# Kernel optimization log

Hardware: AMD Instinct MI355X
Metric: run time of the kernel (lower is better)

Reference implementation:

```python
import jax, jax.numpy as jnp
import numpy as np

B, S = 32, 2048
D = 128      # embedding_dim
H = 256      # hidden_dim
K = 512      # codebook_size
RECON_COEF, COMMIT_COEF, VQ_COEF = 1.0, 0.15, 0.05


def _conv1d(x, w, b):
    # x: [B, Cin, S], w: [Cout, Cin, 3], 'SAME' padding (padding=1, k=3)
    y = jax.lax.conv_general_dilated(x, w, window_strides=(1,), padding='SAME',
                                     dimension_numbers=('NCH', 'OIH', 'NCH'))
    return y + b[None, :, None]


def _lrelu(x):
    return jnp.where(x >= 0, x, 0.2 * x)


def setup_inputs() -> dict:
    key = jax.random.key(0)
    ks = jax.random.split(key, 14)

    def w(k, shape, fan_in):
        bound = 1.0 / np.sqrt(fan_in)
        return jax.random.uniform(k, shape, jnp.float32, -bound, bound)

    return {
        'x': jax.random.normal(ks[0], (B, S), jnp.float32),
        'codebook': jax.random.normal(ks[1], (K, D), jnp.float32),
        'ew1': w(ks[2], (H, 1, 3), 1 * 3),  'eb1': w(ks[3], (H,), 1 * 3),
        'ew2': w(ks[4], (H, H, 3), H * 3),  'eb2': w(ks[5], (H,), H * 3),
        'ew3': w(ks[6], (D, H, 3), H * 3),  'eb3': w(ks[7], (D,), H * 3),
        'dw1': w(ks[8], (H, D, 3), D * 3),  'db1': w(ks[9], (H,), D * 3),
        'dw2': w(ks[10], (H, H, 3), H * 3), 'db2': w(ks[11], (H,), H * 3),
        'dw3': w(ks[12], (1, H, 3), H * 3), 'db3': w(ks[13], (1,), H * 3),
    }


def reference(x, codebook, ew1, eb1, ew2, eb2, ew3, eb3, dw1, db1, dw2, db2, dw3, db3):
    # ---- encode ----
    h = x[:, None, :]                                  # [B,1,S]
    h = _lrelu(_conv1d(h, ew1, eb1))
    h = _lrelu(_conv1d(h, ew2, eb2))
    z = _conv1d(h, ew3, eb3)                           # [B,D,S]

    # ---- vector quantize (eval mode: no EMA update) ----
    zt = jnp.transpose(z, (0, 2, 1))                   # [B,S,D]
    z_flat = zt.reshape(-1, D)                         # [B*S,D]
    # squared distances: |z|^2 + |c|^2 - 2 z c^T
    d = (jnp.sum(z_flat ** 2, axis=1, keepdims=True)
         + jnp.sum(codebook ** 2, axis=1)
         - 2.0 * z_flat @ codebook.T)                  # [B*S,K]
    idx = jnp.argmin(d, axis=1)                        # [B*S]
    z_q = codebook[idx].reshape(zt.shape)              # [B,S,D] (== one-hot @ codebook)

    vq_loss = jnp.mean((jax.lax.stop_gradient(zt) - z_q) ** 2) * VQ_COEF
    commitment_loss = jnp.mean((zt - jax.lax.stop_gradient(z_q)) ** 2) * COMMIT_COEF
    indices = idx.reshape(B, S)

    # ---- decode ----
    h = jnp.transpose(z_q, (0, 2, 1))                  # [B,D,S]
    h = _lrelu(_conv1d(h, dw1, db1))
    h = _lrelu(_conv1d(h, dw2, db2))
    x_recon = _conv1d(h, dw3, db3)[:, 0, :]            # [B,S]

    recon_loss = jnp.mean((x - x_recon) ** 2) * RECON_COEF
    loss = recon_loss + vq_loss + commitment_loss
    return x_recon, indices, loss, recon_loss, vq_loss, commitment_loss
```

## Files before the change

### kernel.cpp

```cpp
#include <hip/hip_runtime.h>
#include <float.h>

#define S_LEN 2048
#define BATCH 32
#define HCH   256
#define DCH   128
#define KCODES 512

typedef float  f32x4  __attribute__((ext_vector_type(4)));
typedef short  bf16x8 __attribute__((ext_vector_type(8)));
typedef short  short8 __attribute__((ext_vector_type(8)));

__device__ __forceinline__ float lrelu_f(float v) { return v >= 0.f ? v : 0.2f * v; }

__device__ __forceinline__ short f2bf(float f) {
    unsigned u = __float_as_uint(f);
    u = u + 0x7fffu + ((u >> 16) & 1u);
    return (short)(u >> 16);
}
__device__ __forceinline__ float bf2f(unsigned short u) {
    return __uint_as_float(((unsigned)u) << 16);
}

__global__ void prep_cb_split_kernel(const float* __restrict__ cb,
                                     short* __restrict__ cb_hi, short* __restrict__ cb_lo,
                                     float* __restrict__ cnorm) {
    int k = blockIdx.x * 256 + threadIdx.x;
    if (k < KCODES) {
        float s = 0.f;
        for (int d = 0; d < DCH; ++d) {
            float v = cb[k * DCH + d];
            s += v * v;
            short hi = f2bf(v);
            short lo = f2bf(v - bf2f((unsigned short)hi));
            cb_hi[k * DCH + d] = hi;
            cb_lo[k * DCH + d] = lo;
        }
        cnorm[k] = s;
    }
}

__global__ void prep_w_split_kernel(const float* __restrict__ Wsrc,
                                    short* __restrict__ Wh, short* __restrict__ Wl,
                                    int Cout, int Cin) {
    int i = blockIdx.x * 256 + threadIdx.x;
    int total = 3 * Cout * Cin;
    if (i < total) {
        int t = i / (Cout * Cin);
        int rem = i - t * Cout * Cin;
        int co = rem / Cin;
        int ci = rem - co * Cin;
        float v = Wsrc[(co * Cin + ci) * 3 + t];
        short hi = f2bf(v);
        Wh[i] = hi;
        Wl[i] = f2bf(v - bf2f((unsigned short)hi));
    }
}

__global__ void prep_wdec_kernel(const float* __restrict__ Wsrc, short* __restrict__ Wdst,
                                 int Cin) {
    int i = blockIdx.x * 256 + threadIdx.x;
    int total = 3 * 256 * Cin;
    if (i < total) {
        int t = i / (256 * Cin);
        int rem = i - t * 256 * Cin;
        int co = rem / Cin;
        int ci = rem - co * Cin;
        Wdst[i] = f2bf(Wsrc[(co * Cin + ci) * 3 + t]);
    }
}

__global__ void prep_w3t_kernel(const float* __restrict__ w3, float* __restrict__ w3t) {
    int i = blockIdx.x * 256 + threadIdx.x;
    if (i < 768) {
        int t = i / 256, ci = i - t * 256;
        w3t[i] = w3[ci * 3 + t];
    }
}

__global__ __launch_bounds__(256) void enc_conv1_cl_kernel(
        const float* __restrict__ x, short* __restrict__ h_hi, short* __restrict__ h_lo,
        const float* __restrict__ w, const float* __restrict__ bias) {
    __shared__ float ws[HCH * 3];
    __shared__ float bs[HCH];
    int tid = threadIdx.x;
    for (int i = tid; i < HCH * 3; i += 256) ws[i] = w[i];
    for (int i = tid; i < HCH; i += 256) bs[i] = bias[i];
    __syncthreads();
    int b = blockIdx.y;
    int s = blockIdx.x * 32 + (tid >> 3);
    int cch = tid & 7;
    const float* xb = x + (size_t)b * S_LEN;
    float xm = (s > 0) ? xb[s - 1] : 0.f;
    float x0 = xb[s];
    float xp = (s < S_LEN - 1) ? xb[s + 1] : 0.f;
    size_t base = ((size_t)(b * S_LEN + s)) * HCH + cch * 32;
#pragma unroll
    for (int cc = 0; cc < 4; ++cc) {
        short8 oh, ol;
#pragma unroll
        for (int e = 0; e < 8; ++e) {
            int co = cch * 32 + cc * 8 + e;
            float v = ws[co * 3 + 0] * xm + ws[co * 3 + 1] * x0 + ws[co * 3 + 2] * xp + bs[co];
            v = lrelu_f(v);
            short hi = f2bf(v);
            oh[e] = hi;
            ol[e] = f2bf(v - bf2f((unsigned short)hi));
        }
        *(short8*)(h_hi + base + cc * 8) = oh;
        *(short8*)(h_lo + base + cc * 8) = ol;
    }
}

__global__ __launch_bounds__(256) void conv_mfma_split(
        const short* __restrict__ in_hi, const short* __restrict__ in_lo,
        short* __restrict__ out_hi, short* __restrict__ out_lo,
        const short* __restrict__ wt_hi, const short* __restrict__ wt_lo,
        const float* __restrict__ bias, int Cin, int Cout, int do_lrelu) {
    __shared__ short smem[20800];
    short* Xh = smem;
    short* Xl = smem + 130 * 40;

    const int tid = threadIdx.x;
    const int lane = tid & 63;
    const int w = tid >> 6;
    const int m = lane & 15;
    const int q = lane >> 4;
    const int sOff = (w & 1) * 64;
    const int cOff = (w >> 1) * 64;
    const int b = blockIdx.z;
    const int s0 = blockIdx.x * 128;
    const int co0 = blockIdx.y * 128;

    f32x4 acc[4][4];
    f32x4 zero4 = {0.f, 0.f, 0.f, 0.f};
#pragma unroll
    for (int i = 0; i < 4; ++i)
#pragma unroll
        for (int j = 0; j < 4; ++j) acc[i][j] = zero4;

    const short* inhb = in_hi + (size_t)b * S_LEN * Cin;
    const short* inlb = in_lo + (size_t)b * S_LEN * Cin;

    for (int ci0 = 0; ci0 < Cin; ci0 += 32) {
        __syncthreads();
        for (int c = tid; c < 520; c += 256) {
            int r = c >> 2, part = c & 3;
            int s = s0 - 1 + r;
            float4 vh = make_float4(0.f, 0.f, 0.f, 0.f);
            float4 vl = vh;
            if (s >= 0 && s < S_LEN) {
                size_t goff = (size_t)s * Cin + ci0 + part * 8;
                vh = *(const float4*)(inhb + goff);
                vl = *(const float4*)(inlb + goff);
            }
            *(float4*)(Xh + r * 40 + part * 8) = vh;
            *(float4*)(Xl + r * 40 + part * 8) = vl;
        }
        __syncthreads();

#pragma unroll
        for (int t = 0; t < 3; ++t) {
            bf16x8 ah[4], al[4], bh[4], bl[4];
#pragma unroll
            for (int i = 0; i < 4; ++i) {
                int row = sOff + i * 16 + m + t;
                ah[i] = *(const bf16x8*)(Xh + row * 40 + q * 8);
                al[i] = *(const bf16x8*)(Xl + row * 40 + q * 8);
            }
#pragma unroll
            for (int j = 0; j < 4; ++j) {
                size_t woff = ((size_t)(t * Cout + co0 + cOff + j * 16 + m)) * Cin + ci0 + q * 8;
                bh[j] = *(const bf16x8*)(wt_hi + woff);
                bl[j] = *(const bf16x8*)(wt_lo + woff);
            }
#pragma unroll
            for (int i = 0; i < 4; ++i)
#pragma unroll
                for (int j = 0; j < 4; ++j) {
                    acc[i][j] = __builtin_amdgcn_mfma_f32_16x16x32_bf16(ah[i], bh[j], acc[i][j], 0, 0, 0);
                    acc[i][j] = __builtin_amdgcn_mfma_f32_16x16x32_bf16(ah[i], bl[j], acc[i][j], 0, 0, 0);
                    acc[i][j] = __builtin_amdgcn_mfma_f32_16x16x32_bf16(al[i], bh[j], acc[i][j], 0, 0, 0);
                }
        }
    }

    short* obH = smem + w * 5120;
    short* obL = obH + 2560;
#pragma unroll
    for (int p = 0; p < 2; ++p) {
        __syncthreads();
#pragma unroll
        for (int jj = 0; jj < 2; ++jj) {
            int j = 2 * p + jj;
            float bv = bias[co0 + cOff + j * 16 + m];
#pragma unroll
            for (int i = 0; i < 4; ++i) {
#pragma unroll
                for (int r = 0; r < 4; ++r) {
                    float val = acc[i][j][r] + bv;
                    if (do_lrelu) val = lrelu_f(val);
                    short hi = f2bf(val);
                    short lo = f2bf(val - bf2f((unsigned short)hi));
                    int row = i * 16 + q * 4 + r;
                    int col = jj * 16 + m;
                    obH[row * 40 + col] = hi;
                    obL[row * 40 + col] = lo;
                }
            }
        }
        __syncthreads();
        const int chunk = lane & 3;
        const int rsub = lane >> 2;
#pragma unroll
        for (int it = 0; it < 4; ++it) {
            int row = it * 16 + rsub;
            short8 vh = *(const short8*)(obH + row * 40 + chunk * 8);
            short8 vl = *(const short8*)(obL + row * 40 + chunk * 8);
            size_t goff = ((size_t)(b * S_LEN + s0 + sOff + row)) * Cout + co0 + cOff + p * 32 + chunk * 8;
            *(short8*)(out_hi + goff) = vh;
            *(short8*)(out_lo + goff) = vl;
        }
    }
}

__global__ __launch_bounds__(256) void vq_mfma_kernel(
        const short* __restrict__ z_hi, const short* __restrict__ z_lo,
        const short* __restrict__ cb_hi, const short* __restrict__ cb_lo,
        const float* __restrict__ cnorm, int* __restrict__ idx_out,
        float* __restrict__ idx_f_out) {
    __shared__ short smem[2 * 64 * 136];
    __shared__ float redv[64][4];
    __shared__ int   redi[64][4];
    short* Zh = smem;
    short* Zl = smem + 64 * 136;

    const int tid = threadIdx.x;
    const int lane = tid & 63;
    const int w = tid >> 6;
    const int m = lane & 15;
    const int q = lane >> 4;
    const int n0 = blockIdx.x * 64;

    for (int c = tid; c < 2048; c += 256) {
        int buf = c >> 10;
        int rem = c & 1023;
        int r = rem >> 4, part = rem & 15;
        size_t goff = (size_t)(n0 + r) * DCH + part * 8;
        float4 v = buf ? *(const float4*)(z_lo + goff) : *(const float4*)(z_hi + goff);
        *(float4*)((buf ? Zl : Zh) + r * 136 + part * 8) = v;
    }
    __syncthreads();

    float best[4][4];
    int besti[4][4];
#pragma unroll
    for (int i = 0; i < 4; ++i)
#pragma unroll
        for (int r = 0; r < 4; ++r) { best[i][r] = FLT_MAX; besti[i][r] = 0; }

    for (int k0 = 0; k0 < KCODES; k0 += 256) {
        f32x4 acc[4][4];
        f32x4 zero4 = {0.f, 0.f, 0.f, 0.f};
#pragma unroll
        for (int i = 0; i < 4; ++i)
#pragma unroll
            for (int j = 0; j < 4; ++j) acc[i][j] = zero4;

#pragma unroll
        for (int d0 = 0; d0 < DCH; d0 += 32) {
            bf16x8 ah[4], al[4], bh[4], bl[4];
#pragma unroll
            for (int i = 0; i < 4; ++i) {
                int row = i * 16 + m;
                ah[i] = *(const bf16x8*)(Zh + row * 136 + d0 + q * 8);
                al[i] = *(const bf16x8*)(Zl + row * 136 + d0 + q * 8);
            }
#pragma unroll
            for (int j = 0; j < 4; ++j) {
                size_t coff = (size_t)(k0 + w * 64 + j * 16 + m) * DCH + d0 + q * 8;
                bh[j] = *(const bf16x8*)(cb_hi + coff);
                bl[j] = *(const bf16x8*)(cb_lo + coff);
            }
#pragma unroll
            for (int i = 0; i < 4; ++i)
#pragma unroll
                for (int j = 0; j < 4; ++j) {
                    acc[i][j] = __builtin_amdgcn_mfma_f32_16x16x32_bf16(ah[i], bh[j], acc[i][j], 0, 0, 0);
                    acc[i][j] = __builtin_amdgcn_mfma_f32_16x16x32_bf16(ah[i], bl[j], acc[i][j], 0, 0, 0);
                    acc[i][j] = __builtin_amdgcn_mfma_f32_16x16x32_bf16(al[i], bh[j], acc[i][j], 0, 0, 0);
                }
        }
#pragma unroll
        for (int j = 0; j < 4; ++j) {
            int k = k0 + w * 64 + j * 16 + m;
            float cn = cnorm[k];
#pragma unroll
            for (int i = 0; i < 4; ++i)
#pragma unroll
                for (int r = 0; r < 4; ++r) {
                    float dv = cn - 2.f * acc[i][j][r];
                    if (dv < best[i][r]) { best[i][r] = dv; besti[i][r] = k; }
                }
        }
    }

#pragma unroll
    for (int mask = 1; mask < 16; mask <<= 1) {
#pragma unroll
        for (int i = 0; i < 4; ++i)
#pragma unroll
            for (int r = 0; r < 4; ++r) {
                float ov = __shfl_xor(best[i][r], mask);
                int oi = __shfl_xor(besti[i][r], mask);
                if (ov < best[i][r] || (ov == best[i][r] && oi < besti[i][r])) {
                    best[i][r] = ov; besti[i][r] = oi;
                }
            }
    }
    if (m == 0) {
#pragma unroll
        for (int i = 0; i < 4; ++i)
#pragma unroll
            for (int r = 0; r < 4; ++r) {
                int srow = i * 16 + q * 4 + r;
                redv[srow][w] = best[i][r];
                redi[srow][w] = besti[i][r];
            }
    }
    __syncthreads();
    if (tid < 64) {
        float bv = redv[tid][0];
        int bi = redi[tid][0];
#pragma unroll
        for (int w2 = 1; w2 < 4; ++w2) {
            float v = redv[tid][w2];
            int ii = redi[tid][w2];
            if (v < bv || (v == bv && ii < bi)) { bv = v; bi = ii; }
        }
        int n = n0 + tid;
        idx_out[n] = bi;
        idx_f_out[n] = (float)bi;
    }
}

__global__ __launch_bounds__(256) void gather_vqsum_kernel(
        const float* __restrict__ cb, const int* __restrict__ idxb,
        const short* __restrict__ z_hi, const short* __restrict__ z_lo,
        short* __restrict__ zq, float* __restrict__ acc_vq) {
    int tid = threadIdx.x;
    int b = blockIdx.y;
    int s = blockIdx.x * 32 + (tid >> 3);
    int dpart = tid & 7;
    int n = b * S_LEN + s;
    int k = idxb[n];
    const float* src = cb + (size_t)k * DCH + dpart * 16;
    size_t zoff = (size_t)n * DCH + dpart * 16;
    float sum = 0.f;
    short8 outv[2];
#pragma unroll
    for (int half = 0; half < 2; ++half) {
        float4 f0 = *(const float4*)(src + half * 8);
        float4 f1 = *(const float4*)(src + half * 8 + 4);
        bf16x8 zh = *(const bf16x8*)(z_hi + zoff + half * 8);
        bf16x8 zl = *(const bf16x8*)(z_lo + zoff + half * 8);
        float qv[8] = {f0.x, f0.y, f0.z, f0.w, f1.x, f1.y, f1.z, f1.w};
        short8 o;
#pragma unroll
        for (int e = 0; e < 8; ++e) {
            o[e] = f2bf(qv[e]);
            float zv = bf2f((unsigned short)zh[e]) + bf2f((unsigned short)zl[e]);
            float df = zv - qv[e];
            sum += df * df;
        }
        outv[half] = o;
    }
    *(short8*)(zq + zoff) = outv[0];
    *(short8*)(zq + zoff + 8) = outv[1];
    for (int off = 32; off > 0; off >>= 1) sum += __shfl_down(sum, off);
    __shared__ float wsum[4];
    if ((tid & 63) == 0) wsum[tid >> 6] = sum;
    __syncthreads();
    if (tid == 0) atomicAdd(acc_vq, wsum[0] + wsum[1] + wsum[2] + wsum[3]);
}

__global__ __launch_bounds__(256) void conv_mfma_cl(
        const short* __restrict__ in, short* __restrict__ out,
        const short* __restrict__ wt, const float* __restrict__ bias,
        int Cin) {
    __shared__ short smem[24672];
    short* Xs = smem;
    short* Ws = smem + 130 * 48;

    const int tid = threadIdx.x;
    const int lane = tid & 63;
    const int w = tid >> 6;
    const int m = lane & 15;
    const int q = lane >> 4;
    const int sOff = (w & 1) * 64;
    const int cOff = (w >> 1) * 64;
    const int b = blockIdx.z;
    const int s0 = blockIdx.x * 128;
    const int co0 = blockIdx.y * 128;

    f32x4 acc[4][4];
    f32x4 zero4 = {0.f, 0.f, 0.f, 0.f};
#pragma unroll
    for (int i = 0; i < 4; ++i)
#pragma unroll
        for (int j = 0; j < 4; ++j) acc[i][j] = zero4;

    const short* inb = in + (size_t)b * S_LEN * Cin;

    for (int ci0 = 0; ci0 < Cin; ci0 += 32) {
        __syncthreads();
        for (int c = tid; c < 520; c += 256) {
            int r = c >> 2, part = c & 3;
            int s = s0 - 1 + r;
            float4 v = make_float4(0.f, 0.f, 0.f, 0.f);
            if (s >= 0 && s < S_LEN)
                v = *(const float4*)(inb + (size_t)s * Cin + ci0 + part * 8);
            *(float4*)(Xs + r * 48 + part * 8) = v;
        }
        for (int c = tid; c < 1536; c += 256) {
            int t = c >> 9;
            int rem = c & 511;
            int cr = rem >> 2, part = rem & 3;
            float4 v = *(const float4*)(wt + ((size_t)(t * 256 + co0 + cr)) * Cin + ci0 + part * 8);
            *(float4*)(Ws + (t * 128 + cr) * 48 + part * 8) = v;
        }
        __syncthreads();

#pragma unroll
        for (int t = 0; t < 3; ++t) {
            bf16x8 a[4], bb[4];
#pragma unroll
            for (int i = 0; i < 4; ++i)
                a[i] = *(const bf16x8*)(Xs + (sOff + i * 16 + m + t) * 48 + q * 8);
#pragma unroll
            for (int j = 0; j < 4; ++j)
                bb[j] = *(const bf16x8*)(Ws + (t * 128 + cOff + j * 16 + m) * 48 + q * 8);
#pragma unroll
            for (int i = 0; i < 4; ++i)
#pragma unroll
                for (int j = 0; j < 4; ++j)
                    acc[i][j] = __builtin_amdgcn_mfma_f32_16x16x32_bf16(
                        a[i], bb[j], acc[i][j], 0, 0, 0);
        }
    }

    __syncthreads();

    short* ob = smem + w * (64 * 80);
#pragma unroll
    for (int j = 0; j < 4; ++j) {
        float bv = bias[co0 + cOff + j * 16 + m];
#pragma unroll
        for (int i = 0; i < 4; ++i) {
#pragma unroll
            for (int r = 0; r < 4; ++r) {
                float val = acc[i][j][r] + bv;
                val = lrelu_f(val);
                ob[(i * 16 + q * 4 + r) * 80 + j * 16 + m] = f2bf(val);
            }
        }
    }
    const int rsel = lane >> 3;
    const int off8 = (lane & 7) * 8;
#pragma unroll
    for (int pass = 0; pass < 8; ++pass) {
        int rr = pass * 8 + rsel;
        short8 v = *(const short8*)(ob + rr * 80 + off8);
        *(short8*)(out + ((size_t)(b * S_LEN + s0 + sOff + rr)) * 256 + co0 + cOff + off8) = v;
    }
}

__global__ __launch_bounds__(256) void dec_conv3_tiled_kernel(
        const short* __restrict__ h, const float* __restrict__ w3t,
        const float* __restrict__ b3, const float* __restrict__ x,
        float* __restrict__ xr, float* __restrict__ acc_recon) {
    __shared__ short Zs[66 * 264];
    __shared__ float ws[3 * 256];
    __shared__ float wsum[4];
    int tid = threadIdx.x;
    int b = blockIdx.y;
    int s0 = blockIdx.x * 64;
    const short* hb = h + (size_t)b * S_LEN * HCH;
    for (int i = tid; i < 768; i += 256) ws[i] = w3t[i];
    for (int c = tid; c < 2112; c += 256) {
        int r = c >> 5, part = c & 31;
        int g = s0 - 1 + r;
        short8 v = {0, 0, 0, 0, 0, 0, 0, 0};
        if (g >= 0 && g < S_LEN)
            v = *(const short8*)(hb + (size_t)g * HCH + part * 8);
        *(short8*)(Zs + r * 264 + part * 8) = v;
    }
    __syncthreads();

    int quarter = tid & 3;
    int sl = tid >> 2;
    float a0 = 0.f, a1 = 0.f, a2 = 0.f, a3 = 0.f;
#pragma unroll
    for (int t = 0; t < 3; ++t) {
        const short* zrow = Zs + (sl + t) * 264 + quarter * 64;
        const float* wrow = ws + t * 256 + quarter * 64;
#pragma unroll
        for (int c = 0; c < 8; ++c) {
            bf16x8 v = *(const bf16x8*)(zrow + c * 8);
            float4 w0 = *(const float4*)(wrow + c * 8);
            float4 w1 = *(const float4*)(wrow + c * 8 + 4);
            a0 = fmaf(w0.x, bf2f((unsigned short)v[0]), a0);
            a1 = fmaf(w0.y, bf2f((unsigned short)v[1]), a1);
            a2 = fmaf(w0.z, bf2f((unsigned short)v[2]), a2);
            a3 = fmaf(w0.w, bf2f((unsigned short)v[3]), a3);
            a0 = fmaf(w1.x, bf2f((unsigned short)v[4]), a0);
            a1 = fmaf(w1.y, bf2f((unsigned short)v[5]), a1);
            a2 = fmaf(w1.z, bf2f((unsigned short)v[6]), a2);
            a3 = fmaf(w1.w, bf2f((unsigned short)v[7]), a3);
        }
    }
    float acc = (a0 + a1) + (a2 + a3);
    acc += __shfl_xor(acc, 1);
    acc += __shfl_xor(acc, 2);
    float df2 = 0.f;
    if (quarter == 0) {
        int s = s0 + sl;
        float tot = acc + b3[0];
        xr[b * S_LEN + s] = tot;
        float df = x[b * S_LEN + s] - tot;
        df2 = df * df;
    }
    for (int off = 32; off > 0; off >>= 1) df2 += __shfl_down(df2, off);
    int lane = tid & 63, wv = tid >> 6;
    if (lane == 0) wsum[wv] = df2;
    __syncthreads();
    if (tid == 0) atomicAdd(acc_recon, wsum[0] + wsum[1] + wsum[2] + wsum[3]);
}

__global__ void finalize_kernel(const float* __restrict__ accs, float* __restrict__ out) {
    if (threadIdx.x == 0) {
        float vqm = accs[0] / ((float)BATCH * S_LEN * DCH);
        float rm  = accs[1] / ((float)BATCH * S_LEN);
        float vq_loss = vqm * 0.05f;
        float commit  = vqm * 0.15f;
        float recon   = rm * 1.0f;
        out[0] = recon + vq_loss + commit;
        out[1] = recon;
        out[2] = vq_loss;
        out[3] = commit;
    }
}

extern "C" void kernel_launch(void* const* d_in, const int* in_sizes, int n_in,
                              void* d_out, int out_size, void* d_ws, size_t ws_size,
                              hipStream_t stream) {
    const float* x    = (const float*)d_in[0];
    const float* cb   = (const float*)d_in[1];
    const float* ew1  = (const float*)d_in[2];
    const float* eb1  = (const float*)d_in[3];
    const float* ew2  = (const float*)d_in[4];
    const float* eb2  = (const float*)d_in[5];
    const float* ew3  = (const float*)d_in[6];
    const float* eb3  = (const float*)d_in[7];
    const float* dw1  = (const float*)d_in[8];
    const float* db1  = (const float*)d_in[9];
    const float* dw2  = (const float*)d_in[10];
    const float* db2  = (const float*)d_in[11];
    const float* dw3  = (const float*)d_in[12];
    const float* db3  = (const float*)d_in[13];

    float* out = (float*)d_out;
    float* xr    = out;
    float* idx_f = out + BATCH * S_LEN;
    float* loss_out = out + 2 * BATCH * S_LEN;

    const size_t NH = (size_t)BATCH * S_LEN * HCH;
    const size_t ND = (size_t)BATCH * S_LEN * DCH;

    short* sp = (short*)d_ws;
    short* h1_hi = sp;
    short* h1_lo = sp + NH;
    short* z_hi  = sp;
    short* z_lo  = sp + ND;
    short* h1d_bf = sp;
    short* h2_hi = sp + 2 * NH;
    short* h2_lo = sp + 3 * NH;
    short* zq_bf = sp + 2 * NH;
    short* h2d_bf = sp + 3 * NH;
    short* sm = sp + 4 * NH;
    short* cb_hi = sm; sm += KCODES * DCH;
    short* cb_lo = sm; sm += KCODES * DCH;
    short* w2_hi = sm; sm += 3 * HCH * HCH;
    short* w2_lo = sm; sm += 3 * HCH * HCH;
    short* w3_hi = sm; sm += 3 * DCH * HCH;
    short* w3_lo = sm; sm += 3 * DCH * HCH;
    short* wbf_d1 = sm; sm += 3 * 256 * DCH;
    short* wbf_d2 = sm; sm += 3 * 256 * HCH;
    float* cnorm = (float*)sm;
    int* idxb = (int*)(cnorm + KCODES);
    float* w3t = (float*)(idxb + BATCH * S_LEN);
    float* accs = w3t + 768;

    hipMemsetAsync(accs, 0, 2 * sizeof(float), stream);

    prep_cb_split_kernel<<<2, 256, 0, stream>>>(cb, cb_hi, cb_lo, cnorm);
    prep_w_split_kernel<<<(3 * HCH * HCH + 255) / 256, 256, 0, stream>>>(ew2, w2_hi, w2_lo, HCH, HCH);
    prep_w_split_kernel<<<(3 * DCH * HCH + 255) / 256, 256, 0, stream>>>(ew3, w3_hi, w3_lo, DCH, HCH);
    prep_wdec_kernel<<<(3 * 256 * DCH + 255) / 256, 256, 0, stream>>>(dw1, wbf_d1, DCH);
    prep_wdec_kernel<<<(3 * 256 * HCH + 255) / 256, 256, 0, stream>>>(dw2, wbf_d2, HCH);
    prep_w3t_kernel<<<3, 256, 0, stream>>>(dw3, w3t);

    enc_conv1_cl_kernel<<<dim3(S_LEN / 32, BATCH), 256, 0, stream>>>(x, h1_hi, h1_lo, ew1, eb1);
    conv_mfma_split<<<dim3(S_LEN / 128, HCH / 128, BATCH), 256, 0, stream>>>(
        h1_hi, h1_lo, h2_hi, h2_lo, w2_hi, w2_lo, eb2, HCH, HCH, 1);
    conv_mfma_split<<<dim3(S_LEN / 128, DCH / 128, BATCH), 256, 0, stream>>>(
        h2_hi, h2_lo, z_hi, z_lo, w3_hi, w3_lo, eb3, HCH, DCH, 0);

    vq_mfma_kernel<<<(BATCH * S_LEN) / 64, 256, 0, stream>>>(
        z_hi, z_lo, cb_hi, cb_lo, cnorm, idxb, idx_f);
    gather_vqsum_kernel<<<dim3(S_LEN / 32, BATCH), 256, 0, stream>>>(
        cb, idxb, z_hi, z_lo, zq_bf, accs);

    conv_mfma_cl<<<dim3(S_LEN / 128, 2, BATCH), 256, 0, stream>>>(
        zq_bf, h1d_bf, wbf_d1, db1, DCH);
    conv_mfma_cl<<<dim3(S_LEN / 128, 2, BATCH), 256, 0, stream>>>(
        h1d_bf, h2d_bf, wbf_d2, db2, HCH);
    dec_conv3_tiled_kernel<<<dim3(S_LEN / 64, BATCH), 256, 0, stream>>>(
        h2d_bf, w3t, db3, x, xr, accs + 1);

    finalize_kernel<<<1, 64, 0, stream>>>(accs, loss_out);
}
```

Measured before the change: 525.1 us.

## Use async global-to-LDS loads with XOR swizzle and 64-channel K steps in conv

The split-bf16 conv kernel now stages input tiles with global_load_lds direct-to-LDS copies into an XOR-swizzled layout, and processes 64 input channels per sync instead of 32. Boundary rows are zero-filled separately. The epilogue is reorganised to write per-16-column chunks through a smaller per-wave LDS buffer, and launch bounds request 4 blocks per SM. The intent is to cut VGPR staging, LDS bank conflicts and barrier count, at the cost of tight wave-lane ordering assumptions for the async copy.

New measurement: 592.4 us. +12.8%, slower.

```diff
diff --git a/kernel.cpp b/kernel.cpp
--- a/kernel.cpp
+++ b/kernel.cpp
@@ -20,6 +20,13 @@
 }
 __device__ __forceinline__ float bf2f(unsigned short u) {
     return __uint_as_float(((unsigned)u) << 16);
+}
+
+__device__ __forceinline__ void async_copy16(short* lds, const short* g) {
+    __builtin_amdgcn_global_load_lds(
+        (const __attribute__((address_space(1))) unsigned int*)g,
+        (__attribute__((address_space(3))) unsigned int*)lds,
+        16, 0, 0);
 }
 
 __global__ void prep_cb_split_kernel(const float* __restrict__ cb,
@@ -112,25 +119,23 @@
     }
 }
 
-__global__ __launch_bounds__(256) void conv_mfma_split(
+__global__ __launch_bounds__(256, 4) void conv_mfma_split(
         const short* __restrict__ in_hi, const short* __restrict__ in_lo,
         short* __restrict__ out_hi, short* __restrict__ out_lo,
         const short* __restrict__ wt_hi, const short* __restrict__ wt_lo,
         const float* __restrict__ bias, int Cin, int Cout, int do_lrelu) {
-    __shared__ short smem[20800];
-    short* Xh = smem;
-    short* Xl = smem + 130 * 40;
-
-    const int tid = threadIdx.x;
+    __shared__ short smem[16640];
+
+    const int tid  = threadIdx.x;
     const int lane = tid & 63;
-    const int w = tid >> 6;
-    const int m = lane & 15;
-    const int q = lane >> 4;
+    const int w    = tid >> 6;
+    const int m    = lane & 15;
+    const int q    = lane >> 4;
     const int sOff = (w & 1) * 64;
     const int cOff = (w >> 1) * 64;
-    const int b = blockIdx.z;
-    const int s0 = blockIdx.x * 128;
-    const int co0 = blockIdx.y * 128;
+    const int b    = blockIdx.z;
+    const int s0   = blockIdx.x * 128;
+    const int co0  = blockIdx.y * 128;
 
     f32x4 acc[4][4];
     f32x4 zero4 = {0.f, 0.f, 0.f, 0.f};
@@ -141,83 +146,94 @@
 
     const short* inhb = in_hi + (size_t)b * S_LEN * Cin;
     const short* inlb = in_lo + (size_t)b * S_LEN * Cin;
-
-    for (int ci0 = 0; ci0 < Cin; ci0 += 32) {
+    const char* XhB = (const char*)smem;
+    const char* XlB = XhB + 1040 * 16;
+
+    for (int ci0 = 0; ci0 < Cin; ci0 += 64) {
         __syncthreads();
-        for (int c = tid; c < 520; c += 256) {
-            int r = c >> 2, part = c & 3;
-            int s = s0 - 1 + r;
-            float4 vh = make_float4(0.f, 0.f, 0.f, 0.f);
-            float4 vl = vh;
-            if (s >= 0 && s < S_LEN) {
-                size_t goff = (size_t)s * Cin + ci0 + part * 8;
-                vh = *(const float4*)(inhb + goff);
-                vl = *(const float4*)(inlb + goff);
+
+        if (s0 == 0 && tid < 16) {
+            short8 z = {0, 0, 0, 0, 0, 0, 0, 0};
+            int buf = tid >> 3, slot = tid & 7;
+            *(short8*)(smem + (size_t)(buf * 1040 + slot) * 8) = z;
+        }
+        if (s0 == S_LEN - 128 && tid < 16) {
+            short8 z = {0, 0, 0, 0, 0, 0, 0, 0};
+            int buf = tid >> 3, slot = tid & 7;
+            *(short8*)(smem + (size_t)(buf * 1040 + 129 * 8 + slot) * 8) = z;
+        }
+
+        for (int c = tid; c < 2080; c += 256) {
+            int base_c = c - lane;
+            int buf  = (c >= 1040) ? 1 : 0;
+            int cc   = c - buf * 1040;
+            int r    = cc >> 3;
+            int slot = cc & 7;
+            int gch  = slot ^ (r & 7);
+            int s    = s0 - 1 + r;
+            short* ldsb = smem + (size_t)base_c * 8;
+            const short* gp = (buf ? inlb : inhb) + (size_t)s * Cin + ci0 + gch * 8;
+            if (s >= 0 && s < S_LEN) async_copy16(ldsb, gp);
+        }
+        __syncthreads();
+
+#pragma unroll
+        for (int ks = 0; ks < 2; ++ks) {
+#pragma unroll
+            for (int t = 0; t < 3; ++t) {
+                bf16x8 ah[4], al[4], bh[4], bl[4];
+#pragma unroll
+                for (int i = 0; i < 4; ++i) {
+                    int row = sOff + i * 16 + m + t;
+                    int off = row * 128 + (((ks * 4 + q) ^ (row & 7)) << 4);
+                    ah[i] = *(const bf16x8*)(XhB + off);
+                    al[i] = *(const bf16x8*)(XlB + off);
+                }
+#pragma unroll
+                for (int j = 0; j < 4; ++j) {
+                    size_t woff = ((size_t)(t * Cout + co0 + cOff + j * 16 + m)) * Cin
+                                  + ci0 + ks * 32 + q * 8;
+                    bh[j] = *(const bf16x8*)(wt_hi + woff);
+                    bl[j] = *(const bf16x8*)(wt_lo + woff);
+                }
+#pragma unroll
+                for (int i = 0; i < 4; ++i)
+#pragma unroll
+                    for (int j = 0; j < 4; ++j) {
+                        acc[i][j] = __builtin_amdgcn_mfma_f32_16x16x32_bf16(ah[i], bh[j], acc[i][j], 0, 0, 0);
+                        acc[i][j] = __builtin_amdgcn_mfma_f32_16x16x32_bf16(ah[i], bl[j], acc[i][j], 0, 0, 0);
+                        acc[i][j] = __builtin_amdgcn_mfma_f32_16x16x32_bf16(al[i], bh[j], acc[i][j], 0, 0, 0);
+                    }
             }
-            *(float4*)(Xh + r * 40 + part * 8) = vh;
-            *(float4*)(Xl + r * 40 + part * 8) = vl;
-        }
-        __syncthreads();
-
-#pragma unroll
-        for (int t = 0; t < 3; ++t) {
-            bf16x8 ah[4], al[4], bh[4], bl[4];
-#pragma unroll
-            for (int i = 0; i < 4; ++i) {
-                int row = sOff + i * 16 + m + t;
-                ah[i] = *(const bf16x8*)(Xh + row * 40 + q * 8);
-                al[i] = *(const bf16x8*)(Xl + row * 40 + q * 8);
+        }
+    }
+
+    __syncthreads();
+
+    short* ob = smem + w * 2560;
+#pragma unroll
+    for (int j = 0; j < 4; ++j) {
+        float bv = bias[co0 + cOff + j * 16 + m];
+#pragma unroll
+        for (int i = 0; i < 4; ++i)
+#pragma unroll
+            for (int r = 0; r < 4; ++r) {
+                float val = acc[i][j][r] + bv;
+                if (do_lrelu) val = lrelu_f(val);
+                short hi = f2bf(val);
+                short lo = f2bf(val - bf2f((unsigned short)hi));
+                int rl = i * 16 + q * 4 + r;
+                ob[rl * 20 + m] = hi;
+                ob[1280 + rl * 20 + m] = lo;
             }
 #pragma unroll
-            for (int j = 0; j < 4; ++j) {
-                size_t woff = ((size_t)(t * Cout + co0 + cOff + j * 16 + m)) * Cin + ci0 + q * 8;
-                bh[j] = *(const bf16x8*)(wt_hi + woff);
-                bl[j] = *(const bf16x8*)(wt_lo + woff);
-            }
-#pragma unroll
-            for (int i = 0; i < 4; ++i)
-#pragma unroll
-                for (int j = 0; j < 4; ++j) {
-                    acc[i][j] = __builtin_amdgcn_mfma_f32_16x16x32_bf16(ah[i], bh[j], acc[i][j], 0, 0, 0);
-                    acc[i][j] = __builtin_amdgcn_mfma_f32_16x16x32_bf16(ah[i], bl[j], acc[i][j], 0, 0, 0);
-                    acc[i][j] = __builtin_amdgcn_mfma_f32_16x16x32_bf16(al[i], bh[j], acc[i][j], 0, 0, 0);
-                }
-        }
-    }
-
-    short* obH = smem + w * 5120;
-    short* obL = obH + 2560;
-#pragma unroll
-    for (int p = 0; p < 2; ++p) {
-        __syncthreads();
-#pragma unroll
-        for (int jj = 0; jj < 2; ++jj) {
-            int j = 2 * p + jj;
-            float bv = bias[co0 + cOff + j * 16 + m];
-#pragma unroll
-            for (int i = 0; i < 4; ++i) {
-#pragma unroll
-                for (int r = 0; r < 4; ++r) {
-                    float val = acc[i][j][r] + bv;
-                    if (do_lrelu) val = lrelu_f(val);
-                    short hi = f2bf(val);
-                    short lo = f2bf(val - bf2f((unsigned short)hi));
-                    int row = i * 16 + q * 4 + r;
-                    int col = jj * 16 + m;
-                    obH[row * 40 + col] = hi;
-                    obL[row * 40 + col] = lo;
-                }
-            }
-        }
-        __syncthreads();
-        const int chunk = lane & 3;
-        const int rsub = lane >> 2;
-#pragma unroll
-        for (int it = 0; it < 4; ++it) {
-            int row = it * 16 + rsub;
-            short8 vh = *(const short8*)(obH + row * 40 + chunk * 8);
-            short8 vl = *(const short8*)(obL + row * 40 + chunk * 8);
-            size_t goff = ((size_t)(b * S_LEN + s0 + sOff + row)) * Cout + co0 + cOff + p * 32 + chunk * 8;
+        for (int itr = 0; itr < 2; ++itr) {
+            int rl = (lane >> 1) + itr * 32;
+            int ch = lane & 1;
+            short8 vh = *(const short8*)(ob + rl * 20 + ch * 8);
+            short8 vl = *(const short8*)(ob + 1280 + rl * 20 + ch * 8);
+            size_t goff = ((size_t)(b * S_LEN + s0 + sOff + rl)) * Cout
+                          + co0 + cOff + j * 16 + ch * 8;
             *(short8*)(out_hi + goff) = vh;
             *(short8*)(out_lo + goff) = vl;
         }
```
